# Performance work log

Hardware: AMD Instinct MI355X
Metric: run time of the kernel (lower is better)

Reference implementation:

```python
import jax, jax.numpy as jnp
import numpy as np

D_MODEL = 768
N_HEADS = 12
HEAD_DIM = D_MODEL // N_HEADS


def setup_inputs() -> dict:
    key = jax.random.key(0)
    ks = jax.random.split(key, 9)
    s = 1.0 / np.sqrt(D_MODEL)
    inp = {
        "inputs": jax.random.normal(ks[0], (1, 4096, D_MODEL), dtype=jnp.float32),
        "Wq": jax.random.uniform(ks[1], (D_MODEL, D_MODEL), jnp.float32, -s, s),
        "bq": jax.random.uniform(ks[2], (D_MODEL,), jnp.float32, -s, s),
        "Wk": jax.random.uniform(ks[3], (D_MODEL, D_MODEL), jnp.float32, -s, s),
        "bk": jax.random.uniform(ks[4], (D_MODEL,), jnp.float32, -s, s),
        "Wv": jax.random.uniform(ks[5], (D_MODEL, D_MODEL), jnp.float32, -s, s),
        "bv": jax.random.uniform(ks[6], (D_MODEL,), jnp.float32, -s, s),
        "Wo": jax.random.uniform(ks[7], (D_MODEL, D_MODEL), jnp.float32, -s, s),
        "bo": jax.random.uniform(ks[8], (D_MODEL,), jnp.float32, -s, s),
    }
    return inp


def reference(inputs, Wq, bq, Wk, bk, Wv, bv, Wo, bo):
    B, S, D = inputs.shape
    H, Hd = N_HEADS, HEAD_DIM

    def split_heads(x):  # [B,S,D] -> [B,H,S,Hd]
        return x.reshape(B, S, H, Hd).transpose(0, 2, 1, 3)

    # nn.Linear computes x @ W.T + b
    Q = split_heads(inputs @ Wq.T + bq)
    K = split_heads(inputs @ Wk.T + bk)
    V = split_heads(inputs @ Wv.T + bv)

    scores = jnp.einsum("bhsd,bhtd->bhst", Q, K) / jnp.sqrt(jnp.float32(Hd))
    causal = jnp.tril(jnp.ones((S, S), dtype=bool))  # True = keep
    scores = jnp.where(causal, scores, -jnp.inf)
    attn = jax.nn.softmax(scores, axis=-1)  # dropout is identity in eval

    out = jnp.einsum("bhst,bhtd->bhsd", attn, V)
    out = out.transpose(0, 2, 1, 3).reshape(B, S, D)
    return out @ Wo.T + bo
```

## Files before the change

### kernel.cpp

```cpp
#include <hip/hip_runtime.h>
#include <stdint.h>

#define SEQ 4096
#define DM 768
#define NH 12
#define HD 64

typedef unsigned short u16;
typedef short short8 __attribute__((ext_vector_type(8)));
typedef float floatx4 __attribute__((ext_vector_type(4)));
typedef float floatx16 __attribute__((ext_vector_type(16)));

__device__ inline u16 f2b(float f) {
  union { float f; uint32_t u; } v; v.f = f;
  uint32_t u = v.u;
  return (u16)((u + 0x7fffu + ((u >> 16) & 1u)) >> 16);
}

__device__ inline float b2f(u16 x) {
  union { uint32_t u; float f; } v; v.u = ((uint32_t)x) << 16;
  return v.f;
}

#if defined(__has_builtin)
#if __has_builtin(__builtin_amdgcn_cvt_pk_bf16_f32)
#define HAVE_PK_BF16 1
#endif
#endif

__device__ inline uint32_t pk_bf16(float a, float b) {
#ifdef HAVE_PK_BF16
  typedef __bf16 bf16x2_t __attribute__((ext_vector_type(2)));
  union { bf16x2_t v; uint32_t u; } c;
  c.v = __builtin_amdgcn_cvt_pk_bf16_f32(a, b);
  return c.u;
#else
  uint32_t r;
  asm("v_cvt_pk_bf16_f32 %0, %1, %2" : "=v"(r) : "v"(a), "v"(b));
  return r;
#endif
}

__device__ inline void pl32swap(uint32_t& a, uint32_t& b) {
  asm("v_permlane32_swap_b32 %0, %1" : "+v"(a), "+v"(b));
}

__device__ inline void load_lds16(const void* g, void* l) {
  __builtin_amdgcn_global_load_lds(
      (const __attribute__((address_space(1))) uint32_t*)g,
      (__attribute__((address_space(3))) uint32_t*)l, 16, 0, 0);
}

__global__ __launch_bounds__(256) void convert_all(
    const float* __restrict__ X, const float* __restrict__ Wq,
    const float* __restrict__ Wk, const float* __restrict__ Wv,
    const float* __restrict__ Wo,
    u16* __restrict__ Xb, u16* __restrict__ Wqb, u16* __restrict__ Wkb,
    u16* __restrict__ Wvb, u16* __restrict__ Wob) {
  int t = blockIdx.x * 256 + threadIdx.x;
  const int NX = SEQ * DM / 4;
  const int NW = DM * DM / 4;
  const float* src; u16* dst; int off;
  if (t < NX)               { src = X;  dst = Xb;  off = t; }
  else if (t < NX + NW)     { src = Wq; dst = Wqb; off = t - NX; }
  else if (t < NX + 2 * NW) { src = Wk; dst = Wkb; off = t - NX - NW; }
  else if (t < NX + 3 * NW) { src = Wv; dst = Wvb; off = t - NX - 2 * NW; }
  else if (t < NX + 4 * NW) { src = Wo; dst = Wob; off = t - NX - 3 * NW; }
  else return;
  float4 v = *(const float4*)(src + (size_t)off * 4);
  uint2 o;
  o.x = pk_bf16(v.x, v.y);
  o.y = pk_bf16(v.z, v.w);
  *(uint2*)(dst + (size_t)off * 4) = o;
}

__global__ __launch_bounds__(128) void gemm_qkv(
    const u16* __restrict__ Xb,
    const u16* __restrict__ Wqb, const u16* __restrict__ Wkb,
    const u16* __restrict__ Wvb,
    const float* __restrict__ bq, const float* __restrict__ bk,
    const float* __restrict__ bv,
    u16* __restrict__ Qh, u16* __restrict__ Kh, u16* __restrict__ VtG) {
  const u16* W; const float* bias;
  const int z = blockIdx.z;
  if (z == 0)      { W = Wqb; bias = bq; }
  else if (z == 1) { W = Wkb; bias = bk; }
  else             { W = Wvb; bias = bv; }

  __shared__ u16 As[2 * 8192];
  __shared__ u16 Bs[2 * 4096];

  const int tid = threadIdx.x;
  const int wave = tid >> 6, lane = tid & 63;
  const int g = lane >> 4, ln = lane & 15;
  const int m0 = blockIdx.y * 128, n0 = blockIdx.x * 64;
  const int srow = lane >> 3;
  const int schunk = (lane & 7) ^ srow;
  const int swz = ln & 7;

  floatx4 acc[4][4] = {};

  auto stage = [&](int k0, int buf) {
#pragma unroll
    for (int i = 0; i < 8; ++i) {
      int u = wave * 8 + i;
      load_lds16(Xb + (size_t)(m0 + u * 8 + srow) * DM + k0 + schunk * 8,
                 As + buf * 8192 + u * 512);
    }
#pragma unroll
    for (int i = 0; i < 4; ++i) {
      int u = wave * 4 + i;
      load_lds16(W + (size_t)(n0 + u * 8 + srow) * DM + k0 + schunk * 8,
                 Bs + buf * 4096 + u * 512);
    }
  };

  stage(0, 0);

  for (int kt = 0; kt < 12; ++kt) {
    const int cur = kt & 1;
    __syncthreads();
    if (kt < 11) stage((kt + 1) * 64, cur ^ 1);
    const u16* Ac = As + cur * 8192;
    const u16* Bc = Bs + cur * 4096;
#pragma unroll
    for (int kh = 0; kh < 2; ++kh) {
      short8 af[4], bf[4];
#pragma unroll
      for (int mi = 0; mi < 4; ++mi)
        af[mi] = *(const short8*)(Ac + (wave * 64 + mi * 16 + ln) * 64 +
                                  ((kh * 4 + g) ^ swz) * 8);
#pragma unroll
      for (int ni = 0; ni < 4; ++ni)
        bf[ni] = *(const short8*)(Bc + (ni * 16 + ln) * 64 +
                                  ((kh * 4 + g) ^ swz) * 8);
#pragma unroll
      for (int mi = 0; mi < 4; ++mi)
#pragma unroll
        for (int ni = 0; ni < 4; ++ni)
          acc[mi][ni] = __builtin_amdgcn_mfma_f32_16x16x32_bf16(
              af[mi], bf[ni], acc[mi][ni], 0, 0, 0);
    }
  }

  const float qscale = 0.125f * 1.44269504089f;
  const int hh = blockIdx.x;
  __syncthreads();

  if (z == 2) {
    u16* ep = (u16*)As;
#pragma unroll
    for (int mi = 0; mi < 4; ++mi) {
      int row0 = wave * 64 + mi * 16 + g * 4;
#pragma unroll
      for (int ni = 0; ni < 4; ++ni) {
        int col = ni * 16 + ln;
        float b = bias[n0 + col];
        uint2 o;
        o.x = pk_bf16(acc[mi][ni][0] + b, acc[mi][ni][1] + b);
        o.y = pk_bf16(acc[mi][ni][2] + b, acc[mi][ni][3] + b);
        *(uint2*)(ep + col * 136 + row0) = o;
      }
    }
    __syncthreads();
#pragma unroll
    for (int t = 0; t < 8; ++t) {
      int unit = tid + t * 128;
      int dcol = unit >> 4, ch = unit & 15;
      short8 v = *(const short8*)(ep + dcol * 136 + ch * 8);
      *(short8*)(VtG + ((size_t)(hh * 64 + dcol)) * SEQ + m0 + ch * 8) = v;
    }
  } else {
    u16* ep = (u16*)As;
    u16* out = (z == 0) ? Qh : Kh;
    float cs = (z == 0) ? qscale : 1.0f;
#pragma unroll
    for (int mi = 0; mi < 4; ++mi) {
      int row0 = wave * 64 + mi * 16 + g * 4;
#pragma unroll
      for (int ni = 0; ni < 4; ++ni) {
        int col = ni * 16 + ln;
        float b = bias[n0 + col];
        uint32_t w0 = pk_bf16((acc[mi][ni][0] + b) * cs, (acc[mi][ni][1] + b) * cs);
        uint32_t w1 = pk_bf16((acc[mi][ni][2] + b) * cs, (acc[mi][ni][3] + b) * cs);
        ep[(row0 + 0) * 72 + col] = (u16)w0;
        ep[(row0 + 1) * 72 + col] = (u16)(w0 >> 16);
        ep[(row0 + 2) * 72 + col] = (u16)w1;
        ep[(row0 + 3) * 72 + col] = (u16)(w1 >> 16);
      }
    }
    __syncthreads();
#pragma unroll
    for (int t = 0; t < 8; ++t) {
      int unit = tid + t * 128;
      int row = unit >> 3, ch = unit & 7;
      short8 v = *(const short8*)(ep + row * 72 + ch * 8);
      *(short8*)(out + ((size_t)hh * SEQ + m0 + row) * HD + ch * 8) = v;
    }
  }
}

#define CHUNK 16
#define M0 40.0f
__global__ __launch_bounds__(256, 4) void attn_chunk(
    const u16* __restrict__ Qh, const u16* __restrict__ Kh,
    const u16* __restrict__ VtG, u16* __restrict__ Opart,
    float* __restrict__ Lp) {
  const int p = blockIdx.y * NH + blockIdx.x;
  const int slot = p % 24, cyc = p / 24;
  const int qq = 3 * (slot & 7) + (slot >> 3);
  const int h = qq >> 1;
  const int b = 79 - (cyc * 2 + (qq & 1));
  int qB, ci;
  if (b < 8)       { qB = b;               ci = 0; }
  else if (b < 24) { int r = b - 8;  qB = 8 + (r >> 1); ci = r & 1; }
  else if (b < 48) { int r = b - 24; int d = r / 3; qB = 16 + d; ci = r - d * 3; }
  else             { int r = b - 48; qB = 24 + (r >> 2); ci = r & 3; }
  const int kb0 = ci * CHUNK;
  const int kb1 = min(kb0 + CHUNK, 2 * qB + 2);
  const int slot2 = (h * 32 + qB) * 4 + ci;

  const int tid = threadIdx.x, wave = tid >> 6, lane = tid & 63;
  const int hi = lane >> 5, lq = lane & 31;
  const int q0 = qB * 128;
  const int qwave = q0 + wave * 32;
  const int srow = lane >> 3;
  const int schunk = (lane & 7) ^ srow;
  const int rsw = lane & 7;

  __shared__ u16 Ks[2 * 4096];
  __shared__ u16 Vt[2 * 4096];

  const int qglob = qwave + lq;
  const u16* Qbase = Qh + ((size_t)h * SEQ + qglob) * HD;
  short8 aq[4];
#pragma unroll
  for (int s = 0; s < 4; ++s)
    aq[s] = *(const short8*)(Qbase + s * 16 + hi * 8);

  floatx16 oacc[2] = {};
  floatx4 lacc = {};

  const size_t kbase = (size_t)h * SEQ * HD;
  const size_t vbase = (size_t)h * 64 * SEQ;

  auto stage = [&](int kbIdx, int buf) {
#pragma unroll
    for (int i = 0; i < 2; ++i) {
      int u = wave * 2 + i;
      load_lds16(Kh + kbase + (size_t)(kbIdx * 64 + u * 8 + srow) * HD + schunk * 8,
                 Ks + buf * 4096 + u * 512);
      load_lds16(VtG + vbase + (size_t)(u * 8 + srow) * SEQ + kbIdx * 64 + schunk * 8,
                 Vt + buf * 4096 + u * 512);
    }
  };

  stage(kb0, 0);

  for (int kb = kb0; kb < kb1; ++kb) {
    const int cur = (kb - kb0) & 1;
    __syncthreads();
    if (kb + 1 < kb1) stage(kb + 1, cur ^ 1);

    const u16* Kc = Ks + cur * 4096;
    const u16* Vc = Vt + cur * 4096;

    if (kb * 64 > qwave + 31) continue;

    floatx16 st[2];
#pragma unroll
    for (int kblk = 0; kblk < 2; ++kblk)
#pragma unroll
      for (int r2 = 0; r2 < 16; ++r2) st[kblk][r2] = -M0;
    __builtin_amdgcn_s_setprio(1);
#pragma unroll
    for (int s = 0; s < 4; ++s)
#pragma unroll
      for (int kblk = 0; kblk < 2; ++kblk) {
        short8 kf = *(const short8*)(Kc + (kblk * 32 + lq) * 64 +
                                     ((s * 2 + hi) ^ rsw) * 8);
        st[kblk] = __builtin_amdgcn_mfma_f32_32x32x16_bf16(kf, aq[s], st[kblk],
                                                           0, 0, 0);
      }
    __builtin_amdgcn_s_setprio(0);

    if (kb * 64 + 63 > qwave) {
#pragma unroll
      for (int kblk = 0; kblk < 2; ++kblk)
#pragma unroll
        for (int r2 = 0; r2 < 16; ++r2) {
          int key = kb * 64 + kblk * 32 + (r2 & 3) + 8 * (r2 >> 2) + 4 * hi;
          if (key > qglob) st[kblk][r2] = -1e30f;
        }
    }

    uint32_t w[2][8];
#pragma unroll
    for (int kblk = 0; kblk < 2; ++kblk) {
#pragma unroll
      for (int r2 = 0; r2 < 16; ++r2)
        st[kblk][r2] = __builtin_amdgcn_exp2f(st[kblk][r2]);
#pragma unroll
      for (int r2 = 0; r2 < 4; ++r2)
        lacc[r2] += st[kblk][r2] + st[kblk][4 + r2] + st[kblk][8 + r2] +
                    st[kblk][12 + r2];
#pragma unroll
      for (int i = 0; i < 8; ++i)
        w[kblk][i] = pk_bf16(st[kblk][2 * i], st[kblk][2 * i + 1]);
    }

    __builtin_amdgcn_s_setprio(1);
#pragma unroll
    for (int ks = 0; ks < 4; ++ks) {
      const int kblk = ks >> 1, base = (ks & 1) * 4;
      uint32_t d0 = w[kblk][base + 0], d2 = w[kblk][base + 2];
      uint32_t d1 = w[kblk][base + 1], d3 = w[kblk][base + 3];
      pl32swap(d0, d2);
      pl32swap(d1, d3);
      union { uint32_t u[4]; short8 s; } bp;
      bp.u[0] = d0; bp.u[1] = d1; bp.u[2] = d2; bp.u[3] = d3;
#pragma unroll
      for (int dblk = 0; dblk < 2; ++dblk) {
        short8 vf = *(const short8*)(Vc + (dblk * 32 + lq) * 64 +
                                     ((ks * 2 + hi) ^ rsw) * 8);
        oacc[dblk] = __builtin_amdgcn_mfma_f32_32x32x16_bf16(vf, bp.s, oacc[dblk],
                                                             0, 0, 0);
      }
    }
    __builtin_amdgcn_s_setprio(0);
  }

  float l_i = lacc[0] + lacc[1] + lacc[2] + lacc[3];
  l_i += __shfl_xor(l_i, 32);

  float inv = 1.f / l_i;
  int qloc = wave * 32 + lq;
  u16* Op = Opart + (size_t)slot2 * 8192 + qloc * 64;
#pragma unroll
  for (int dblk = 0; dblk < 2; ++dblk)
#pragma unroll
    for (int qd = 0; qd < 4; ++qd) {
      uint2 o;
      o.x = pk_bf16(oacc[dblk][qd * 4 + 0] * inv, oacc[dblk][qd * 4 + 1] * inv);
      o.y = pk_bf16(oacc[dblk][qd * 4 + 2] * inv, oacc[dblk][qd * 4 + 3] * inv);
      *(uint2*)(Op + dblk * 32 + qd * 8 + hi * 4) = o;
    }
  if (hi == 0) Lp[(size_t)slot2 * 128 + qloc] = l_i;
}

__global__ __launch_bounds__(256) void attn_merge(
    const u16* __restrict__ Opart, const float* __restrict__ Lp,
    u16* __restrict__ Ob) {
  const int h = blockIdx.x, qB = blockIdx.y;
  const int n = (qB >> 3) + 1;
  const int base = (h * 32 + qB) * 4;
  const int q = threadIdx.x >> 1;
  const int d0 = (threadIdx.x & 1) * 32;

  float L = 0.f;
  for (int i = 0; i < n; ++i) L += Lp[(size_t)(base + i) * 128 + q];
  float invL = 1.f / L;

  float acc[32];
#pragma unroll
  for (int jj = 0; jj < 32; ++jj) acc[jj] = 0.f;
  for (int i = 0; i < n; ++i) {
    float wi = Lp[(size_t)(base + i) * 128 + q] * invL;
    const u16* src = Opart + (size_t)(base + i) * 8192 + q * 64 + d0;
#pragma unroll
    for (int c = 0; c < 4; ++c) {
      short8 a = ((const short8*)src)[c];
#pragma unroll
      for (int jj = 0; jj < 8; ++jj) acc[c * 8 + jj] += wi * b2f((u16)a[jj]);
    }
  }

  u16* dst = Ob + (size_t)(qB * 128 + q) * DM + h * HD + d0;
#pragma unroll
  for (int c = 0; c < 4; ++c) {
    uint4 o;
    o.x = pk_bf16(acc[c * 8 + 0], acc[c * 8 + 1]);
    o.y = pk_bf16(acc[c * 8 + 2], acc[c * 8 + 3]);
    o.z = pk_bf16(acc[c * 8 + 4], acc[c * 8 + 5]);
    o.w = pk_bf16(acc[c * 8 + 6], acc[c * 8 + 7]);
    ((uint4*)dst)[c] = o;
  }
}

__global__ __launch_bounds__(128) void gemm_out(
    const u16* __restrict__ Ab, const u16* __restrict__ Wob,
    const float* __restrict__ bo, float* __restrict__ Cout) {
  __shared__ u16 As[2 * 8192];
  __shared__ u16 Bs[2 * 4096];

  const int tid = threadIdx.x;
  const int wave = tid >> 6, lane = tid & 63;
  const int g = lane >> 4, ln = lane & 15;
  const int m0 = blockIdx.y * 128, n0 = blockIdx.x * 64;
  const int srow = lane >> 3;
  const int schunk = (lane & 7) ^ srow;
  const int swz = ln & 7;

  floatx4 acc[4][4] = {};

  auto stage = [&](int k0, int buf) {
#pragma unroll
    for (int i = 0; i < 8; ++i) {
      int u = wave * 8 + i;
      load_lds16(Ab + (size_t)(m0 + u * 8 + srow) * DM + k0 + schunk * 8,
                 As + buf * 8192 + u * 512);
    }
#pragma unroll
    for (int i = 0; i < 4; ++i) {
      int u = wave * 4 + i;
      load_lds16(Wob + (size_t)(n0 + u * 8 + srow) * DM + k0 + schunk * 8,
                 Bs + buf * 4096 + u * 512);
    }
  };

  stage(0, 0);

  for (int kt = 0; kt < 12; ++kt) {
    const int cur = kt & 1;
    __syncthreads();
    if (kt < 11) stage((kt + 1) * 64, cur ^ 1);
    const u16* Ac = As + cur * 8192;
    const u16* Bc = Bs + cur * 4096;
#pragma unroll
    for (int kh = 0; kh < 2; ++kh) {
      short8 af[4], bf[4];
#pragma unroll
      for (int mi = 0; mi < 4; ++mi)
        af[mi] = *(const short8*)(Ac + (wave * 64 + mi * 16 + ln) * 64 +
                                  ((kh * 4 + g) ^ swz) * 8);
#pragma unroll
      for (int ni = 0; ni < 4; ++ni)
        bf[ni] = *(const short8*)(Bc + (ni * 16 + ln) * 64 +
                                  ((kh * 4 + g) ^ swz) * 8);
#pragma unroll
      for (int mi = 0; mi < 4; ++mi)
#pragma unroll
        for (int ni = 0; ni < 4; ++ni)
          acc[mi][ni] = __builtin_amdgcn_mfma_f32_16x16x32_bf16(
              af[mi], bf[ni], acc[mi][ni], 0, 0, 0);
    }
  }

#pragma unroll
  for (int mi = 0; mi < 4; ++mi) {
    int row = m0 + wave * 64 + mi * 16 + g * 4;
#pragma unroll
    for (int ni = 0; ni < 4; ++ni) {
      int col = n0 + ni * 16 + ln;
      float b = bo[col];
#pragma unroll
      for (int r = 0; r < 4; ++r)
        Cout[(size_t)(row + r) * DM + col] = acc[mi][ni][r] + b;
    }
  }
}

extern "C" void kernel_launch(void* const* d_in, const int* in_sizes, int n_in,
                              void* d_out, int out_size, void* d_ws, size_t ws_size,
                              hipStream_t stream) {
  const float* X  = (const float*)d_in[0];
  const float* Wq = (const float*)d_in[1];
  const float* bq = (const float*)d_in[2];
  const float* Wk = (const float*)d_in[3];
  const float* bk = (const float*)d_in[4];
  const float* Wv = (const float*)d_in[5];
  const float* bv = (const float*)d_in[6];
  const float* Wo = (const float*)d_in[7];
  const float* bo = (const float*)d_in[8];
  float* out = (float*)d_out;

  char* ws = (char*)d_ws;
  u16* Wob = (u16*)ws; ws += (size_t)DM * DM * 2;
  u16* Qh  = (u16*)ws; ws += (size_t)NH * SEQ * HD * 2;
  u16* Kh  = (u16*)ws; ws += (size_t)NH * SEQ * HD * 2;
  u16* VtG = (u16*)ws; ws += (size_t)NH * SEQ * HD * 2;
  u16* Ob  = (u16*)ws; ws += (size_t)SEQ * DM * 2;
  float* Lp = (float*)ws; ws += (size_t)NH * 32 * 4 * 128 * 4;
  char* ovl = ws;
  u16* Xb  = (u16*)ovl;
  u16* Wqb = Xb + (size_t)SEQ * DM;
  u16* Wkb = Wqb + (size_t)DM * DM;
  u16* Wvb = Wkb + (size_t)DM * DM;
  u16* Opart = (u16*)ovl;

  convert_all<<<5376, 256, 0, stream>>>(X, Wq, Wk, Wv, Wo, Xb, Wqb, Wkb, Wvb, Wob);

  dim3 gq(DM / 64, SEQ / 128, 3);
  gemm_qkv<<<gq, 128, 0, stream>>>(Xb, Wqb, Wkb, Wvb, bq, bk, bv, Qh, Kh, VtG);

  dim3 ga(NH, 80);
  attn_chunk<<<ga, 256, 0, stream>>>(Qh, Kh, VtG, Opart, Lp);

  dim3 gm(NH, 32);
  attn_merge<<<gm, 256, 0, stream>>>(Opart, Lp, Ob);

  dim3 go(DM / 64, SEQ / 128);
  gemm_out<<<go, 128, 0, stream>>>(Ob, Wob, bo, out);
}
```

Before: 180.8 us.

## Retile QKV and output GEMMs with larger QKV tiles and smaller output tiles

The QKV GEMM moves to 128x128 tiles with 4 waves in a 2x2 wave layout. It uses a 1D grid with a swizzled block-to-tile mapping across 8 groups, and its epilogue writes two heads per block. The output GEMM moves to 64x64 tiles with 4 waves, giving more blocks so the CUs fill better for that small GEMM. The intent is more operand reuse in the QKV projection and better occupancy and load balance in the output projection. The costs are more shared memory per QKV block and less reuse per block in the output GEMM.

```diff
diff --git a/kernel.cpp b/kernel.cpp
--- a/kernel.cpp
+++ b/kernel.cpp
@@ -74,26 +74,33 @@
   *(uint2*)(dst + (size_t)off * 4) = o;
 }
 
-__global__ __launch_bounds__(128) void gemm_qkv(
+__global__ __launch_bounds__(256) void gemm_qkv(
     const u16* __restrict__ Xb,
     const u16* __restrict__ Wqb, const u16* __restrict__ Wkb,
     const u16* __restrict__ Wvb,
     const float* __restrict__ bq, const float* __restrict__ bk,
     const float* __restrict__ bv,
     u16* __restrict__ Qh, u16* __restrict__ Kh, u16* __restrict__ VtG) {
+  const int p = blockIdx.x;
+  const int wg = (p & 7) * 72 + (p >> 3);
+  const int mb = wg / 18, nz = wg % 18;
+  const int z = nz / 6;
+  const int n0 = (nz % 6) * 128;
+  const int m0 = mb * 128;
+
   const u16* W; const float* bias;
-  const int z = blockIdx.z;
   if (z == 0)      { W = Wqb; bias = bq; }
   else if (z == 1) { W = Wkb; bias = bk; }
   else             { W = Wvb; bias = bv; }
 
-  __shared__ u16 As[2 * 8192];
-  __shared__ u16 Bs[2 * 4096];
+  __shared__ u16 smem[32768];
+  u16* As = smem;
+  u16* Bs = smem + 16384;
 
   const int tid = threadIdx.x;
   const int wave = tid >> 6, lane = tid & 63;
   const int g = lane >> 4, ln = lane & 15;
-  const int m0 = blockIdx.y * 128, n0 = blockIdx.x * 64;
+  const int wm = (wave & 1) * 64, wn = (wave >> 1) * 64;
   const int srow = lane >> 3;
   const int schunk = (lane & 7) ^ srow;
   const int swz = ln & 7;
@@ -102,16 +109,12 @@
 
   auto stage = [&](int k0, int buf) {
 #pragma unroll
-    for (int i = 0; i < 8; ++i) {
-      int u = wave * 8 + i;
+    for (int i = 0; i < 4; ++i) {
+      int u = wave * 4 + i;
       load_lds16(Xb + (size_t)(m0 + u * 8 + srow) * DM + k0 + schunk * 8,
                  As + buf * 8192 + u * 512);
-    }
-#pragma unroll
-    for (int i = 0; i < 4; ++i) {
-      int u = wave * 4 + i;
       load_lds16(W + (size_t)(n0 + u * 8 + srow) * DM + k0 + schunk * 8,
-                 Bs + buf * 4096 + u * 512);
+                 Bs + buf * 8192 + u * 512);
     }
   };
 
@@ -122,17 +125,17 @@
     __syncthreads();
     if (kt < 11) stage((kt + 1) * 64, cur ^ 1);
     const u16* Ac = As + cur * 8192;
-    const u16* Bc = Bs + cur * 4096;
+    const u16* Bc = Bs + cur * 8192;
 #pragma unroll
     for (int kh = 0; kh < 2; ++kh) {
       short8 af[4], bf[4];
 #pragma unroll
       for (int mi = 0; mi < 4; ++mi)
-        af[mi] = *(const short8*)(Ac + (wave * 64 + mi * 16 + ln) * 64 +
+        af[mi] = *(const short8*)(Ac + (wm + mi * 16 + ln) * 64 +
                                   ((kh * 4 + g) ^ swz) * 8);
 #pragma unroll
       for (int ni = 0; ni < 4; ++ni)
-        bf[ni] = *(const short8*)(Bc + (ni * 16 + ln) * 64 +
+        bf[ni] = *(const short8*)(Bc + (wn + ni * 16 + ln) * 64 +
                                   ((kh * 4 + g) ^ swz) * 8);
 #pragma unroll
       for (int mi = 0; mi < 4; ++mi)
@@ -144,17 +147,17 @@
   }
 
   const float qscale = 0.125f * 1.44269504089f;
-  const int hh = blockIdx.x;
+  const int hh0 = n0 >> 6;
   __syncthreads();
+  u16* ep = smem;
 
   if (z == 2) {
-    u16* ep = (u16*)As;
 #pragma unroll
     for (int mi = 0; mi < 4; ++mi) {
-      int row0 = wave * 64 + mi * 16 + g * 4;
+      int row0 = wm + mi * 16 + g * 4;
 #pragma unroll
       for (int ni = 0; ni < 4; ++ni) {
-        int col = ni * 16 + ln;
+        int col = wn + ni * 16 + ln;
         float b = bias[n0 + col];
         uint2 o;
         o.x = pk_bf16(acc[mi][ni][0] + b, acc[mi][ni][1] + b);
@@ -165,37 +168,38 @@
     __syncthreads();
 #pragma unroll
     for (int t = 0; t < 8; ++t) {
-      int unit = tid + t * 128;
+      int unit = tid + t * 256;
       int dcol = unit >> 4, ch = unit & 15;
+      int head = hh0 + (dcol >> 6), d = dcol & 63;
       short8 v = *(const short8*)(ep + dcol * 136 + ch * 8);
-      *(short8*)(VtG + ((size_t)(hh * 64 + dcol)) * SEQ + m0 + ch * 8) = v;
+      *(short8*)(VtG + ((size_t)(head * 64 + d)) * SEQ + m0 + ch * 8) = v;
     }
   } else {
-    u16* ep = (u16*)As;
     u16* out = (z == 0) ? Qh : Kh;
     float cs = (z == 0) ? qscale : 1.0f;
 #pragma unroll
     for (int mi = 0; mi < 4; ++mi) {
-      int row0 = wave * 64 + mi * 16 + g * 4;
+      int row0 = wm + mi * 16 + g * 4;
 #pragma unroll
       for (int ni = 0; ni < 4; ++ni) {
-        int col = ni * 16 + ln;
+        int col = wn + ni * 16 + ln;
         float b = bias[n0 + col];
         uint32_t w0 = pk_bf16((acc[mi][ni][0] + b) * cs, (acc[mi][ni][1] + b) * cs);
         uint32_t w1 = pk_bf16((acc[mi][ni][2] + b) * cs, (acc[mi][ni][3] + b) * cs);
-        ep[(row0 + 0) * 72 + col] = (u16)w0;
-        ep[(row0 + 1) * 72 + col] = (u16)(w0 >> 16);
-        ep[(row0 + 2) * 72 + col] = (u16)w1;
-        ep[(row0 + 3) * 72 + col] = (u16)(w1 >> 16);
+        ep[(row0 + 0) * 136 + col] = (u16)w0;
+        ep[(row0 + 1) * 136 + col] = (u16)(w0 >> 16);
+        ep[(row0 + 2) * 136 + col] = (u16)w1;
+        ep[(row0 + 3) * 136 + col] = (u16)(w1 >> 16);
       }
     }
     __syncthreads();
 #pragma unroll
     for (int t = 0; t < 8; ++t) {
-      int unit = tid + t * 128;
-      int row = unit >> 3, ch = unit & 7;
-      short8 v = *(const short8*)(ep + row * 72 + ch * 8);
-      *(short8*)(out + ((size_t)hh * SEQ + m0 + row) * HD + ch * 8) = v;
+      int unit = tid + t * 256;
+      int row = unit >> 4, ch = unit & 15;
+      int head = hh0 + (ch >> 3), d0 = (ch & 7) * 8;
+      short8 v = *(const short8*)(ep + row * 136 + ch * 8);
+      *(short8*)(out + ((size_t)head * SEQ + m0 + row) * HD + d0) = v;
     }
   }
 }
@@ -387,71 +391,75 @@
   }
 }
 
-__global__ __launch_bounds__(128) void gemm_out(
+__global__ __launch_bounds__(256) void gemm_out(
     const u16* __restrict__ Ab, const u16* __restrict__ Wob,
     const float* __restrict__ bo, float* __restrict__ Cout) {
-  __shared__ u16 As[2 * 8192];
-  __shared__ u16 Bs[2 * 4096];
+  __shared__ u16 smem[16384];
 
   const int tid = threadIdx.x;
   const int wave = tid >> 6, lane = tid & 63;
   const int g = lane >> 4, ln = lane & 15;
-  const int m0 = blockIdx.y * 128, n0 = blockIdx.x * 64;
+  const int m0 = blockIdx.y * 64, n0 = blockIdx.x * 64;
+  const int wm = (wave & 1) * 32, wn = (wave >> 1) * 32;
   const int srow = lane >> 3;
   const int schunk = (lane & 7) ^ srow;
   const int swz = ln & 7;
 
-  floatx4 acc[4][4] = {};
-
-  auto stage = [&](int k0, int buf) {
-#pragma unroll
-    for (int i = 0; i < 8; ++i) {
-      int u = wave * 8 + i;
-      load_lds16(Ab + (size_t)(m0 + u * 8 + srow) * DM + k0 + schunk * 8,
-                 As + buf * 8192 + u * 512);
-    }
-#pragma unroll
-    for (int i = 0; i < 4; ++i) {
-      int u = wave * 4 + i;
-      load_lds16(Wob + (size_t)(n0 + u * 8 + srow) * DM + k0 + schunk * 8,
-                 Bs + buf * 4096 + u * 512);
-    }
-  };
-
-  stage(0, 0);
+  floatx4 acc[2][2] = {};
+
+#pragma unroll
+  for (int i = 0; i < 2; ++i) {
+    int u = wave * 2 + i;
+    load_lds16(Ab + (size_t)(m0 + u * 8 + srow) * DM + schunk * 8, smem + u * 512);
+    load_lds16(Wob + (size_t)(n0 + u * 8 + srow) * DM + schunk * 8,
+               smem + 8192 + u * 512);
+  }
 
   for (int kt = 0; kt < 12; ++kt) {
     const int cur = kt & 1;
     __syncthreads();
-    if (kt < 11) stage((kt + 1) * 64, cur ^ 1);
-    const u16* Ac = As + cur * 8192;
-    const u16* Bc = Bs + cur * 4096;
-#pragma unroll
-    for (int kh = 0; kh < 2; ++kh) {
-      short8 af[4], bf[4];
-#pragma unroll
-      for (int mi = 0; mi < 4; ++mi)
-        af[mi] = *(const short8*)(Ac + (wave * 64 + mi * 16 + ln) * 64 +
-                                  ((kh * 4 + g) ^ swz) * 8);
-#pragma unroll
-      for (int ni = 0; ni < 4; ++ni)
-        bf[ni] = *(const short8*)(Bc + (ni * 16 + ln) * 64 +
-                                  ((kh * 4 + g) ^ swz) * 8);
-#pragma unroll
-      for (int mi = 0; mi < 4; ++mi)
-#pragma unroll
-        for (int ni = 0; ni < 4; ++ni)
+    if (kt < 11) {
+      const int k0 = (kt + 1) * 64, nb = cur ^ 1;
+#pragma unroll
+      for (int i = 0; i < 2; ++i) {
+        int u = wave * 2 + i;
+        load_lds16(Ab + (size_t)(m0 + u * 8 + srow) * DM + k0 + schunk * 8,
+                   smem + nb * 4096 + u * 512);
+        load_lds16(Wob + (size_t)(n0 + u * 8 + srow) * DM + k0 + schunk * 8,
+                   smem + 8192 + nb * 4096 + u * 512);
+      }
+    }
+    const u16* Ac = smem + cur * 4096;
+    const u16* Bc = smem + 8192 + cur * 4096;
+    short8 af[2][2], bf[2][2];
+#pragma unroll
+    for (int mi = 0; mi < 2; ++mi)
+#pragma unroll
+      for (int kh = 0; kh < 2; ++kh)
+        af[mi][kh] = *(const short8*)(Ac + (wm + mi * 16 + ln) * 64 +
+                                      ((kh * 4 + g) ^ swz) * 8);
+#pragma unroll
+    for (int ni = 0; ni < 2; ++ni)
+#pragma unroll
+      for (int kh = 0; kh < 2; ++kh)
+        bf[ni][kh] = *(const short8*)(Bc + (wn + ni * 16 + ln) * 64 +
+                                      ((kh * 4 + g) ^ swz) * 8);
+#pragma unroll
+    for (int kh = 0; kh < 2; ++kh)
+#pragma unroll
+      for (int mi = 0; mi < 2; ++mi)
+#pragma unroll
+        for (int ni = 0; ni < 2; ++ni)
           acc[mi][ni] = __builtin_amdgcn_mfma_f32_16x16x32_bf16(
-              af[mi], bf[ni], acc[mi][ni], 0, 0, 0);
-    }
-  }
-
-#pragma unroll
-  for (int mi = 0; mi < 4; ++mi) {
-    int row = m0 + wave * 64 + mi * 16 + g * 4;
-#pragma unroll
-    for (int ni = 0; ni < 4; ++ni) {
-      int col = n0 + ni * 16 + ln;
+              af[mi][kh], bf[ni][kh], acc[mi][ni], 0, 0, 0);
+  }
+
+#pragma unroll
+  for (int mi = 0; mi < 2; ++mi) {
+    int row = m0 + wm + mi * 16 + g * 4;
+#pragma unroll
+    for (int ni = 0; ni < 2; ++ni) {
+      int col = n0 + wn + ni * 16 + ln;
       float b = bo[col];
 #pragma unroll
       for (int r = 0; r < 4; ++r)
@@ -490,8 +498,7 @@
 
   convert_all<<<5376, 256, 0, stream>>>(X, Wq, Wk, Wv, Wo, Xb, Wqb, Wkb, Wvb, Wob);
 
-  dim3 gq(DM / 64, SEQ / 128, 3);
-  gemm_qkv<<<gq, 128, 0, stream>>>(Xb, Wqb, Wkb, Wvb, bq, bk, bv, Qh, Kh, VtG);
+  gemm_qkv<<<576, 256, 0, stream>>>(Xb, Wqb, Wkb, Wvb, bq, bk, bv, Qh, Kh, VtG);
 
   dim3 ga(NH, 80);
   attn_chunk<<<ga, 256, 0, stream>>>(Qh, Kh, VtG, Opart, Lp);
@@ -499,6 +506,6 @@
   dim3 gm(NH, 32);
   attn_merge<<<gm, 256, 0, stream>>>(Opart, Lp, Ob);
 
-  dim3 go(DM / 64, SEQ / 128);
-  gemm_out<<<go, 128, 0, stream>>>(Ob, Wob, bo, out);
-}
+  dim3 go(DM / 64, SEQ / 64);
+  gemm_out<<<go, 256, 0, stream>>>(Ob, Wob, bo, out);
+}
```

New measurement: 166.2 us. 1.09x faster.
